# Performance work log

Hardware: AMD Instinct MI355X
Metric: run time of the kernel (lower is better)

Reference implementation:

```python
import jax, jax.numpy as jnp
import numpy as np


def _dwconv3x3(x, w, b):
    # depthwise 3x3, stride 1, padding 1 (groups == channels)
    y = jax.lax.conv_general_dilated(
        x, w, window_strides=(1, 1), padding=((1, 1), (1, 1)),
        dimension_numbers=('NCHW', 'OIHW', 'NCHW'),
        feature_group_count=x.shape[1])
    return y + b[None, :, None, None]


def _maxpool(x, f):
    # adaptive_max_pool2d to (h//f, w//f) with h,w divisible by f == stride-f max pool
    return jax.lax.reduce_window(x, -jnp.inf, jax.lax.max,
                                 (1, 1, f, f), (1, 1, f, f), 'VALID')


def _up_nearest(x, f):
    return jnp.repeat(jnp.repeat(x, f, axis=2), f, axis=3)


def setup_inputs() -> dict:
    key = jax.random.key(0)
    ks = jax.random.split(key, 10)
    B, C, H, W = 4, 32, 128, 128
    x = jax.random.normal(ks[0], (B, C, H, W), dtype=jnp.float32)
    mk = lambda k, shape, s: jax.random.normal(k, shape, dtype=jnp.float32) * s
    return {
        'x': x,
        'w0': mk(ks[1], (C, 1, 3, 3), 0.3), 'b0': mk(ks[2], (C,), 0.05),
        'w1': mk(ks[3], (C, 1, 3, 3), 0.3), 'b1': mk(ks[4], (C,), 0.05),
        'w2': mk(ks[5], (C, 1, 3, 3), 0.3), 'b2': mk(ks[6], (C,), 0.05),
        'wa': mk(ks[7], (C, C, 1, 1), 0.2), 'ba': mk(ks[8], (C,), 0.05),
    }


def reference(x, w0, b0, w1, b1, w2, b2, wa, ba):
    b, c, h, w = x.shape
    # multi-scale depthwise feature refinement
    s0 = _dwconv3x3(x, w0, b0)                               # level 0: full res
    s1 = _up_nearest(_dwconv3x3(_maxpool(x, 2), w1, b1), 2)  # level 1: /2
    s2 = _up_nearest(_dwconv3x3(_maxpool(x, 4), w2, b2), 4)  # level 2: /4
    # Channel_mixing8: q=s0, k=s1, v=s2; per-pixel CxC outer product
    to_nc = lambda t: t.transpose(0, 2, 3, 1).reshape(-1, c)  # (N, C), N=b*h*w
    q, k, v = to_nc(s0), to_nc(s1), to_nc(s2)
    kv = v[:, :, None] * k[:, None, :]        # (N, C, C) = v_embed @ k_embed^T
    attn = jax.nn.softmax(kv, axis=1)         # softmax over dim=1 (v axis)
    qkv = jnp.einsum('nij,nj->ni', attn, q)   # matvec with q
    out = qkv.reshape(b, h, w, c).transpose(0, 3, 1, 2)
    # aggr: 1x1 conv; drop_path=0 -> identity
    out = jnp.einsum('bchw,oc->bohw', out, wa[:, :, 0, 0]) + ba[None, :, None, None]
    return jax.nn.gelu(out, approximate=False) * x
```

## Files before the change

kernel.cpp:

```cpp
#include <hip/hip_runtime.h>
#include <math.h>

#define CC 32

__global__ __launch_bounds__(256, 2) void fused_safm(
    const float* __restrict__ x,
    const float* __restrict__ w0, const float* __restrict__ b0,
    const float* __restrict__ w1, const float* __restrict__ b1,
    const float* __restrict__ w2, const float* __restrict__ b2,
    const float* __restrict__ wa, const float* __restrict__ ba,
    float* __restrict__ out) {
  int bid = blockIdx.x;
  int tw = bid & 7;
  int th = (bid >> 3) & 63;
  int b  = bid >> 9;
  int t  = threadIdx.x;
  int h4  = th >> 1;
  int dth = (th & 1) * 2;
  int R0 = 4 * h4 - 4;
  int C0 = 16 * tw - 4;

  __shared__ __align__(16) float smA[11520];
  float* xs   = smA;
  float* p1s  = smA + 9600;
  float* p2s  = smA + 10848;
  float* Ebuf = smA;
  float* scT  = smA + 8288;
  __shared__ __align__(16) float s0s[1056];
  __shared__ __align__(16) float c1s[264];
  __shared__ __align__(16) float vsh[288];
  __shared__ __align__(16) float qkvs[1056];

  {
    int c = t >> 3, sub = t & 7;
    const float* xc = x + ((size_t)(b * CC + c) << 14);
    float* xd = xs + c * 300;
#pragma unroll
    for (int r = 0; r < 12; ++r) {
      int row = R0 + r;
      bool rok = (unsigned)row < 128u;
#pragma unroll
      for (int m = 0; m < 3; ++m) {
        int col = sub * 3 + m;
        int gcol = C0 + col;
        float v = 0.f;
        if (rok && (unsigned)gcol < 128u) v = xc[row * 128 + gcol];
        xd[r * 25 + col] = v;
      }
    }
  }
  __syncthreads();

  for (int k = 0; k < 4; ++k) {
    int idx = t + k * 256;
    if (idx < 960) {
      int c = idx / 30, rem = idx % 30;
      int hp = rem / 10, wp = rem % 10;
      int prow = th - 1 + hp, pcol = 8 * tw - 1 + wp;
      float v = 0.f;
      if ((unsigned)prow < 64u && (unsigned)pcol < 64u) {
        const float* xp = xs + c * 300 + (dth + 2 * hp + 2) * 25 + (2 * wp + 2);
        v = fmaxf(fmaxf(xp[0], xp[1]), fmaxf(xp[25], xp[26]));
      }
      p1s[c * 39 + hp * 13 + wp] = v;
    }
  }
  for (int k = 0; k < 3; ++k) {
    int idx = t + k * 256;
    if (idx < 576) {
      int c = idx / 18, rem = idx % 18;
      int hq = rem / 6, wq = rem % 6;
      int prow = h4 - 1 + hq, pcol = 4 * tw - 1 + wq;
      float v = 0.f;
      if ((unsigned)prow < 32u && (unsigned)pcol < 32u) {
        const float* xp = xs + c * 300 + (4 * hq) * 25 + 4 * wq;
        float m0 = fmaxf(fmaxf(xp[0],  xp[1]),  fmaxf(xp[2],  xp[3]));
        float m1 = fmaxf(fmaxf(xp[25], xp[26]), fmaxf(xp[27], xp[28]));
        float m2 = fmaxf(fmaxf(xp[50], xp[51]), fmaxf(xp[52], xp[53]));
        float m3 = fmaxf(fmaxf(xp[75], xp[76]), fmaxf(xp[77], xp[78]));
        v = fmaxf(fmaxf(m0, m1), fmaxf(m2, m3));
      }
      p2s[c * 21 + hq * 7 + wq] = v;
    }
  }
  __syncthreads();

  {
    int c = t >> 3, gg = t & 7;
    const float* wc = w0 + c * 9;
    float wv[9];
#pragma unroll
    for (int q = 0; q < 9; ++q) wv[q] = wc[q];
    float bz = b0[c];
    int hh = gg >> 2, wb = (gg & 3) * 4;
#pragma unroll
    for (int k = 0; k < 4; ++k) {
      int ww = wb + k;
      const float* xp = xs + c * 300 + (dth + hh + 3) * 25 + (ww + 3);
      float acc = bz;
      acc = fmaf(wv[0], xp[0],  fmaf(wv[1], xp[1],  fmaf(wv[2], xp[2],  acc)));
      acc = fmaf(wv[3], xp[25], fmaf(wv[4], xp[26], fmaf(wv[5], xp[27], acc)));
      acc = fmaf(wv[6], xp[50], fmaf(wv[7], xp[51], fmaf(wv[8], xp[52], acc)));
      s0s[(hh * 16 + ww) * 33 + c] = acc;
    }
  }
  {
    int eb = t >> 5, j = t & 31;
    {
      const float* wc = w1 + j * 9;
      const float* pp = p1s + j * 39 + eb;
      float acc = b1[j];
      acc = fmaf(wc[0], pp[0],  fmaf(wc[1], pp[1],  fmaf(wc[2], pp[2],  acc)));
      acc = fmaf(wc[3], pp[13], fmaf(wc[4], pp[14], fmaf(wc[5], pp[15], acc)));
      acc = fmaf(wc[6], pp[26], fmaf(wc[7], pp[27], fmaf(wc[8], pp[28], acc)));
      c1s[eb * 33 + j] = acc;
    }
    {
      const float* wc = w2 + j * 9;
      const float* pp = p2s + j * 21 + (eb >> 1);
      float acc = b2[j];
      acc = fmaf(wc[0], pp[0],  fmaf(wc[1], pp[1],  fmaf(wc[2], pp[2],  acc)));
      acc = fmaf(wc[3], pp[7],  fmaf(wc[4], pp[8],  fmaf(wc[5], pp[9],  acc)));
      acc = fmaf(wc[6], pp[14], fmaf(wc[7], pp[15], fmaf(wc[8], pp[16], acc)));
      vsh[eb * 36 + j] = acc;
    }
  }
  __syncthreads();

  {
    int eb = t >> 5, j = t & 31;
    float kj = c1s[eb * 33 + j];
    float vv[32];
    const float4* v4 = (const float4*)(vsh + eb * 36);
#pragma unroll
    for (int iq = 0; iq < 8; ++iq) {
      float4 q_ = v4[iq];
      vv[4 * iq] = q_.x; vv[4 * iq + 1] = q_.y; vv[4 * iq + 2] = q_.z; vv[4 * iq + 3] = q_.w;
    }
    float vmax = vv[0], vmin = vv[0];
#pragma unroll
    for (int i = 1; i < CC; ++i) {
      vmax = fmaxf(vmax, vv[i]);
      vmin = fminf(vmin, vv[i]);
    }
    const float L2E = 1.4426950408889634f;
    float m  = (kj >= 0.f) ? kj * vmax : kj * vmin;
    float kl = kj * L2E;
    float nm = -m * L2E;
    float d0 = 0.f, d1 = 0.f, d2 = 0.f, d3 = 0.f;
    float* Ecol = Ebuf + eb * 1036 + j;
#pragma unroll
    for (int i = 0; i < CC; i += 4) {
      float e0 = __builtin_amdgcn_exp2f(fmaf(vv[i],     kl, nm)); Ecol[i * 32]       = e0; d0 += e0;
      float e1 = __builtin_amdgcn_exp2f(fmaf(vv[i + 1], kl, nm)); Ecol[(i + 1) * 32] = e1; d1 += e1;
      float e2 = __builtin_amdgcn_exp2f(fmaf(vv[i + 2], kl, nm)); Ecol[(i + 2) * 32] = e2; d2 += e2;
      float e3 = __builtin_amdgcn_exp2f(fmaf(vv[i + 3], kl, nm)); Ecol[(i + 3) * 32] = e3; d3 += e3;
    }
    float rd = __fdividef(1.f, (d0 + d1) + (d2 + d3));
#pragma unroll
    for (int px = 0; px < 4; ++px) {
      int hh = px >> 1, wwb = px & 1;
      int p = hh * 16 + eb * 2 + wwb;
      scT[j * 33 + p] = s0s[p * 33 + j] * rd;
    }
  }
  __syncthreads();

  {
    int p = t & 31, ic = t >> 5;
    int eb = (p & 15) >> 1;
    const float* Er = Ebuf + eb * 1036 + ic * 128;
    float a0 = 0.f, a1 = 0.f, a2 = 0.f, a3 = 0.f;
#pragma unroll
    for (int jq = 0; jq < 8; ++jq) {
      float4 e0 = *(const float4*)(Er + jq * 4);
      float4 e1 = *(const float4*)(Er + 32 + jq * 4);
      float4 e2 = *(const float4*)(Er + 64 + jq * 4);
      float4 e3 = *(const float4*)(Er + 96 + jq * 4);
      float s0v = scT[(jq * 4)     * 33 + p];
      float s1v = scT[(jq * 4 + 1) * 33 + p];
      float s2v = scT[(jq * 4 + 2) * 33 + p];
      float s3v = scT[(jq * 4 + 3) * 33 + p];
      a0 = fmaf(e0.x, s0v, fmaf(e0.y, s1v, fmaf(e0.z, s2v, fmaf(e0.w, s3v, a0))));
      a1 = fmaf(e1.x, s0v, fmaf(e1.y, s1v, fmaf(e1.z, s2v, fmaf(e1.w, s3v, a1))));
      a2 = fmaf(e2.x, s0v, fmaf(e2.y, s1v, fmaf(e2.z, s2v, fmaf(e2.w, s3v, a2))));
      a3 = fmaf(e3.x, s0v, fmaf(e3.y, s1v, fmaf(e3.z, s2v, fmaf(e3.w, s3v, a3))));
    }
    int i0 = ic * 4;
    qkvs[p * 33 + i0]     = a0;
    qkvs[p * 33 + i0 + 1] = a1;
    qkvs[p * 33 + i0 + 2] = a2;
    qkvs[p * 33 + i0 + 3] = a3;
  }
  __syncthreads();

  {
    int o = t >> 3, g = t & 7;
    int hh = g >> 2, wb = (g & 3) * 4;
    const float* wo = wa + o * 32;
    const float* q0 = qkvs + (hh * 16 + wb)     * 33;
    const float* q1 = qkvs + (hh * 16 + wb + 1) * 33;
    const float* q2 = qkvs + (hh * 16 + wb + 2) * 33;
    const float* q3 = qkvs + (hh * 16 + wb + 3) * 33;
    float bz = ba[o];
    float y0 = bz, y1 = bz, y2 = bz, y3 = bz;
#pragma unroll
    for (int i = 0; i < 32; ++i) {
      float w = wo[i];
      y0 = fmaf(w, q0[i], y0);
      y1 = fmaf(w, q1[i], y1);
      y2 = fmaf(w, q2[i], y2);
      y3 = fmaf(w, q3[i], y3);
    }
    const float RS2 = 0.70710678118654752f;
    float g0 = 0.5f * y0 * (1.f + erff(y0 * RS2));
    float g1 = 0.5f * y1 * (1.f + erff(y1 * RS2));
    float g2 = 0.5f * y2 * (1.f + erff(y2 * RS2));
    float g3 = 0.5f * y3 * (1.f + erff(y3 * RS2));
    size_t ob = (((size_t)(b * CC + o) * 128) + (2 * th + hh)) * 128 + 16 * tw + wb;
    float4 xv = *(const float4*)(x + ob);
    float4 r;
    r.x = g0 * xv.x; r.y = g1 * xv.y; r.z = g2 * xv.z; r.w = g3 * xv.w;
    *(float4*)(out + ob) = r;
  }
}

extern "C" void kernel_launch(void* const* d_in, const int* in_sizes, int n_in,
                              void* d_out, int out_size, void* d_ws, size_t ws_size,
                              hipStream_t stream) {
  const float* x  = (const float*)d_in[0];
  const float* w0 = (const float*)d_in[1];
  const float* b0 = (const float*)d_in[2];
  const float* w1 = (const float*)d_in[3];
  const float* b1 = (const float*)d_in[4];
  const float* w2 = (const float*)d_in[5];
  const float* b2 = (const float*)d_in[6];
  const float* wa = (const float*)d_in[7];
  const float* ba = (const float*)d_in[8];
  float* out = (float*)d_out;

  fused_safm<<<2048, 256, 0, stream>>>(x, w0, b0, w1, b1, w2, b2, wa, ba, out);
}
```

Before: 120.5 us.

## Drop shared x tile, derive pool4 from pool2, store softmax weights as fp16

Stops staging the 12x25 input halo tile per channel in shared memory. Level-1 pooling now reads x straight from global with float2 loads, the full-res depthwise conv reads x rows directly, and level-2 pooling is taken as the max over the level-1 pool buffer. The normalized softmax weights are packed to half2 in shared memory and the matvec reads them as fp16 pairs, and the launch-bounds occupancy hint rises from 2 to 5 blocks. This shrinks LDS use and one barrier to allow more resident blocks, at the cost of more, partly redundant, global loads and fp16 rounding of the attention weights.

```diff
diff --git a/kernel.cpp b/kernel.cpp
--- a/kernel.cpp
+++ b/kernel.cpp
@@ -1,9 +1,18 @@
 #include <hip/hip_runtime.h>
+#include <hip/hip_fp16.h>
 #include <math.h>
 
-#define CC 32
-
-__global__ __launch_bounds__(256, 2) void fused_safm(
+
+__device__ __forceinline__ float2 h2f2(unsigned int u) {
+  __half2 h = *reinterpret_cast<__half2*>(&u);
+  return __half22float2(h);
+}
+__device__ __forceinline__ unsigned int f2h2(float a, float b) {
+  __half2 h = __floats2half2_rn(a, b);
+  return *reinterpret_cast<unsigned int*>(&h);
+}
+
+__global__ __launch_bounds__(256, 5) void fused_safm(
     const float* __restrict__ x,
     const float* __restrict__ w0, const float* __restrict__ b0,
     const float* __restrict__ w1, const float* __restrict__ b1,
@@ -11,127 +20,99 @@
     const float* __restrict__ wa, const float* __restrict__ ba,
     float* __restrict__ out) {
   int bid = blockIdx.x;
-  int tw = bid & 7;
-  int th = (bid >> 3) & 63;
-  int b  = bid >> 9;
-  int t  = threadIdx.x;
-  int h4  = th >> 1;
-  int dth = (th & 1) * 2;
-  int R0 = 4 * h4 - 4;
-  int C0 = 16 * tw - 4;
-
-  __shared__ __align__(16) float smA[11520];
-  float* xs   = smA;
-  float* p1s  = smA + 9600;
-  float* p2s  = smA + 10848;
-  float* Ebuf = smA;
-  float* scT  = smA + 8288;
+  int tw = bid & 7, th = (bid >> 3) & 63, b = bid >> 9;
+  int t = threadIdx.x;
+  int h4 = th >> 1;
+
+  __shared__ __align__(16) unsigned int regA[4128];
   __shared__ __align__(16) float s0s[1056];
-  __shared__ __align__(16) float c1s[264];
   __shared__ __align__(16) float vsh[288];
   __shared__ __align__(16) float qkvs[1056];
-
-  {
-    int c = t >> 3, sub = t & 7;
-    const float* xc = x + ((size_t)(b * CC + c) << 14);
-    float* xd = xs + c * 300;
-#pragma unroll
-    for (int r = 0; r < 12; ++r) {
-      int row = R0 + r;
-      bool rok = (unsigned)row < 128u;
-#pragma unroll
-      for (int m = 0; m < 3; ++m) {
-        int col = sub * 3 + m;
-        int gcol = C0 + col;
-        float v = 0.f;
-        if (rok && (unsigned)gcol < 128u) v = xc[row * 128 + gcol];
-        xd[r * 25 + col] = v;
+  float* p1s = (float*)regA;
+
+  {
+#pragma unroll
+    for (int kk = 0; kk < 9; ++kk) {
+      int idx = t + kk * 256;
+      int c = idx / 72, rem = idx % 72;
+      int r = rem / 12, w = rem % 12;
+      int pr = 2 * h4 - 2 + r, pc = 8 * tw - 2 + w;
+      float v = 0.f;
+      if ((unsigned)pr < 64u && (unsigned)pc < 64u) {
+        const float* xp = x + ((size_t)(b * 32 + c) << 14) + 2 * pr * 128 + 2 * pc;
+        float2 r0 = *(const float2*)xp;
+        float2 r1 = *(const float2*)(xp + 128);
+        v = fmaxf(fmaxf(r0.x, r0.y), fmaxf(r1.x, r1.y));
       }
-    }
-  }
-  __syncthreads();
-
-  for (int k = 0; k < 4; ++k) {
-    int idx = t + k * 256;
-    if (idx < 960) {
-      int c = idx / 30, rem = idx % 30;
-      int hp = rem / 10, wp = rem % 10;
-      int prow = th - 1 + hp, pcol = 8 * tw - 1 + wp;
-      float v = 0.f;
-      if ((unsigned)prow < 64u && (unsigned)pcol < 64u) {
-        const float* xp = xs + c * 300 + (dth + 2 * hp + 2) * 25 + (2 * wp + 2);
-        v = fmaxf(fmaxf(xp[0], xp[1]), fmaxf(xp[25], xp[26]));
-      }
-      p1s[c * 39 + hp * 13 + wp] = v;
-    }
-  }
-  for (int k = 0; k < 3; ++k) {
-    int idx = t + k * 256;
-    if (idx < 576) {
-      int c = idx / 18, rem = idx % 18;
-      int hq = rem / 6, wq = rem % 6;
-      int prow = h4 - 1 + hq, pcol = 4 * tw - 1 + wq;
-      float v = 0.f;
-      if ((unsigned)prow < 32u && (unsigned)pcol < 32u) {
-        const float* xp = xs + c * 300 + (4 * hq) * 25 + 4 * wq;
-        float m0 = fmaxf(fmaxf(xp[0],  xp[1]),  fmaxf(xp[2],  xp[3]));
-        float m1 = fmaxf(fmaxf(xp[25], xp[26]), fmaxf(xp[27], xp[28]));
-        float m2 = fmaxf(fmaxf(xp[50], xp[51]), fmaxf(xp[52], xp[53]));
-        float m3 = fmaxf(fmaxf(xp[75], xp[76]), fmaxf(xp[77], xp[78]));
-        v = fmaxf(fmaxf(m0, m1), fmaxf(m2, m3));
-      }
-      p2s[c * 21 + hq * 7 + wq] = v;
-    }
-  }
-  __syncthreads();
-
+      p1s[c * 73 + r * 12 + w] = v;
+    }
+  }
   {
     int c = t >> 3, gg = t & 7;
+    int hh = gg >> 2, wb = (gg & 3) * 4;
+    const float* xp = x + ((size_t)(b * 32 + c) << 14);
     const float* wc = w0 + c * 9;
     float wv[9];
 #pragma unroll
     for (int q = 0; q < 9; ++q) wv[q] = wc[q];
     float bz = b0[c];
-    int hh = gg >> 2, wb = (gg & 3) * 4;
-#pragma unroll
-    for (int k = 0; k < 4; ++k) {
-      int ww = wb + k;
-      const float* xp = xs + c * 300 + (dth + hh + 3) * 25 + (ww + 3);
-      float acc = bz;
-      acc = fmaf(wv[0], xp[0],  fmaf(wv[1], xp[1],  fmaf(wv[2], xp[2],  acc)));
-      acc = fmaf(wv[3], xp[25], fmaf(wv[4], xp[26], fmaf(wv[5], xp[27], acc)));
-      acc = fmaf(wv[6], xp[50], fmaf(wv[7], xp[51], fmaf(wv[8], xp[52], acc)));
-      s0s[(hh * 16 + ww) * 33 + c] = acc;
-    }
-  }
-  {
-    int eb = t >> 5, j = t & 31;
-    {
-      const float* wc = w1 + j * 9;
-      const float* pp = p1s + j * 39 + eb;
-      float acc = b1[j];
-      acc = fmaf(wc[0], pp[0],  fmaf(wc[1], pp[1],  fmaf(wc[2], pp[2],  acc)));
-      acc = fmaf(wc[3], pp[13], fmaf(wc[4], pp[14], fmaf(wc[5], pp[15], acc)));
-      acc = fmaf(wc[6], pp[26], fmaf(wc[7], pp[27], fmaf(wc[8], pp[28], acc)));
-      c1s[eb * 33 + j] = acc;
-    }
-    {
-      const float* wc = w2 + j * 9;
-      const float* pp = p2s + j * 21 + (eb >> 1);
-      float acc = b2[j];
-      acc = fmaf(wc[0], pp[0],  fmaf(wc[1], pp[1],  fmaf(wc[2], pp[2],  acc)));
-      acc = fmaf(wc[3], pp[7],  fmaf(wc[4], pp[8],  fmaf(wc[5], pp[9],  acc)));
-      acc = fmaf(wc[6], pp[14], fmaf(wc[7], pp[15], fmaf(wc[8], pp[16], acc)));
-      vsh[eb * 36 + j] = acc;
-    }
-  }
-  __syncthreads();
-
-  {
-    int eb = t >> 5, j = t & 31;
-    float kj = c1s[eb * 33 + j];
+    float a0 = bz, a1 = bz, a2 = bz, a3 = bz;
+    int cbase = 16 * tw + wb;
+#pragma unroll
+    for (int dr = -1; dr <= 1; ++dr) {
+      int row = 2 * th + hh + dr;
+      if ((unsigned)row >= 128u) continue;
+      const float* rp = xp + row * 128 + cbase;
+      float cm1 = (cbase > 0)       ? rp[-1] : 0.f;
+      float4 c03 = *(const float4*)rp;
+      float c4  = (cbase + 4 < 128) ? rp[4]  : 0.f;
+      float wA = wv[(dr + 1) * 3], wB = wv[(dr + 1) * 3 + 1], wC = wv[(dr + 1) * 3 + 2];
+      a0 = fmaf(wA, cm1,   fmaf(wB, c03.x, fmaf(wC, c03.y, a0)));
+      a1 = fmaf(wA, c03.x, fmaf(wB, c03.y, fmaf(wC, c03.z, a1)));
+      a2 = fmaf(wA, c03.y, fmaf(wB, c03.z, fmaf(wC, c03.w, a2)));
+      a3 = fmaf(wA, c03.z, fmaf(wB, c03.w, fmaf(wC, c4,    a3)));
+    }
+    int pb = hh * 16 + wb;
+    s0s[(pb)     * 33 + c] = a0;
+    s0s[(pb + 1) * 33 + c] = a1;
+    s0s[(pb + 2) * 33 + c] = a2;
+    s0s[(pb + 3) * 33 + c] = a3;
+  }
+  __syncthreads();
+
+  int ebT = t >> 5, jT = t & 31;
+  float kreg;
+  {
+    const float* wc = w1 + jT * 9;
+    const float* Pk = p1s + jT * 73 + ((th & 1) + 1) * 12 + ebT + 1;
+    float acc = b1[jT];
+    acc = fmaf(wc[0], Pk[0],  fmaf(wc[1], Pk[1],  fmaf(wc[2], Pk[2],  acc)));
+    acc = fmaf(wc[3], Pk[12], fmaf(wc[4], Pk[13], fmaf(wc[5], Pk[14], acc)));
+    acc = fmaf(wc[6], Pk[24], fmaf(wc[7], Pk[25], fmaf(wc[8], Pk[26], acc)));
+    kreg = acc;
+  }
+  {
+    const float* wc = w2 + jT * 9;
+    const float* P = p1s + jT * 73;
+    int cb0 = 2 * (ebT >> 1);
+    float acc = b2[jT];
+#pragma unroll
+    for (int hq = 0; hq < 3; ++hq) {
+      const float* Pr = P + 2 * hq * 12;
+#pragma unroll
+      for (int wq = 0; wq < 3; ++wq) {
+        int cb = cb0 + 2 * wq;
+        float p2v = fmaxf(fmaxf(Pr[cb], Pr[cb + 1]), fmaxf(Pr[cb + 12], Pr[cb + 13]));
+        acc = fmaf(wc[hq * 3 + wq], p2v, acc);
+      }
+    }
+    vsh[ebT * 36 + jT] = acc;
+  }
+  __syncthreads();
+
+  {
     float vv[32];
-    const float4* v4 = (const float4*)(vsh + eb * 36);
+    const float4* v4 = (const float4*)(vsh + ebT * 36);
 #pragma unroll
     for (int iq = 0; iq < 8; ++iq) {
       float4 q_ = v4[iq];
@@ -139,58 +120,55 @@
     }
     float vmax = vv[0], vmin = vv[0];
 #pragma unroll
-    for (int i = 1; i < CC; ++i) {
+    for (int i = 1; i < 32; ++i) {
       vmax = fmaxf(vmax, vv[i]);
       vmin = fminf(vmin, vv[i]);
     }
     const float L2E = 1.4426950408889634f;
-    float m  = (kj >= 0.f) ? kj * vmax : kj * vmin;
-    float kl = kj * L2E;
+    float m  = (kreg >= 0.f) ? kreg * vmax : kreg * vmin;
+    float kl = kreg * L2E;
     float nm = -m * L2E;
+    float e[32];
     float d0 = 0.f, d1 = 0.f, d2 = 0.f, d3 = 0.f;
-    float* Ecol = Ebuf + eb * 1036 + j;
-#pragma unroll
-    for (int i = 0; i < CC; i += 4) {
-      float e0 = __builtin_amdgcn_exp2f(fmaf(vv[i],     kl, nm)); Ecol[i * 32]       = e0; d0 += e0;
-      float e1 = __builtin_amdgcn_exp2f(fmaf(vv[i + 1], kl, nm)); Ecol[(i + 1) * 32] = e1; d1 += e1;
-      float e2 = __builtin_amdgcn_exp2f(fmaf(vv[i + 2], kl, nm)); Ecol[(i + 2) * 32] = e2; d2 += e2;
-      float e3 = __builtin_amdgcn_exp2f(fmaf(vv[i + 3], kl, nm)); Ecol[(i + 3) * 32] = e3; d3 += e3;
+#pragma unroll
+    for (int i = 0; i < 32; i += 4) {
+      e[i]     = __builtin_amdgcn_exp2f(fmaf(vv[i],     kl, nm)); d0 += e[i];
+      e[i + 1] = __builtin_amdgcn_exp2f(fmaf(vv[i + 1], kl, nm)); d1 += e[i + 1];
+      e[i + 2] = __builtin_amdgcn_exp2f(fmaf(vv[i + 2], kl, nm)); d2 += e[i + 2];
+      e[i + 3] = __builtin_amdgcn_exp2f(fmaf(vv[i + 3], kl, nm)); d3 += e[i + 3];
     }
     float rd = __fdividef(1.f, (d0 + d1) + (d2 + d3));
-#pragma unroll
-    for (int px = 0; px < 4; ++px) {
-      int hh = px >> 1, wwb = px & 1;
-      int p = hh * 16 + eb * 2 + wwb;
-      scT[j * 33 + p] = s0s[p * 33 + j] * rd;
-    }
+    unsigned int* EB = regA + ebT * 516 + jT;
+#pragma unroll
+    for (int ip = 0; ip < 16; ++ip)
+      EB[ip * 32] = f2h2(e[2 * ip] * rd, e[2 * ip + 1] * rd);
   }
   __syncthreads();
 
   {
     int p = t & 31, ic = t >> 5;
     int eb = (p & 15) >> 1;
-    const float* Er = Ebuf + eb * 1036 + ic * 128;
+    const unsigned int* EB = regA + eb * 516;
+    const float* qrow = s0s + p * 33;
     float a0 = 0.f, a1 = 0.f, a2 = 0.f, a3 = 0.f;
 #pragma unroll
-    for (int jq = 0; jq < 8; ++jq) {
-      float4 e0 = *(const float4*)(Er + jq * 4);
-      float4 e1 = *(const float4*)(Er + 32 + jq * 4);
-      float4 e2 = *(const float4*)(Er + 64 + jq * 4);
-      float4 e3 = *(const float4*)(Er + 96 + jq * 4);
-      float s0v = scT[(jq * 4)     * 33 + p];
-      float s1v = scT[(jq * 4 + 1) * 33 + p];
-      float s2v = scT[(jq * 4 + 2) * 33 + p];
-      float s3v = scT[(jq * 4 + 3) * 33 + p];
-      a0 = fmaf(e0.x, s0v, fmaf(e0.y, s1v, fmaf(e0.z, s2v, fmaf(e0.w, s3v, a0))));
-      a1 = fmaf(e1.x, s0v, fmaf(e1.y, s1v, fmaf(e1.z, s2v, fmaf(e1.w, s3v, a1))));
-      a2 = fmaf(e2.x, s0v, fmaf(e2.y, s1v, fmaf(e2.z, s2v, fmaf(e2.w, s3v, a2))));
-      a3 = fmaf(e3.x, s0v, fmaf(e3.y, s1v, fmaf(e3.z, s2v, fmaf(e3.w, s3v, a3))));
-    }
-    int i0 = ic * 4;
-    qkvs[p * 33 + i0]     = a0;
-    qkvs[p * 33 + i0 + 1] = a1;
-    qkvs[p * 33 + i0 + 2] = a2;
-    qkvs[p * 33 + i0 + 3] = a3;
+    for (int jw = 0; jw < 8; ++jw) {
+      uint4 wA = *(const uint4*)(EB + (2 * ic)     * 32 + jw * 4);
+      uint4 wB = *(const uint4*)(EB + (2 * ic + 1) * 32 + jw * 4);
+      float q0 = qrow[4 * jw], q1 = qrow[4 * jw + 1];
+      float q2 = qrow[4 * jw + 2], q3 = qrow[4 * jw + 3];
+      float2 f;
+      f = h2f2(wA.x); a0 = fmaf(f.x, q0, a0); a1 = fmaf(f.y, q0, a1);
+      f = h2f2(wA.y); a0 = fmaf(f.x, q1, a0); a1 = fmaf(f.y, q1, a1);
+      f = h2f2(wA.z); a0 = fmaf(f.x, q2, a0); a1 = fmaf(f.y, q2, a1);
+      f = h2f2(wA.w); a0 = fmaf(f.x, q3, a0); a1 = fmaf(f.y, q3, a1);
+      f = h2f2(wB.x); a2 = fmaf(f.x, q0, a2); a3 = fmaf(f.y, q0, a3);
+      f = h2f2(wB.y); a2 = fmaf(f.x, q1, a2); a3 = fmaf(f.y, q1, a3);
+      f = h2f2(wB.z); a2 = fmaf(f.x, q2, a2); a3 = fmaf(f.y, q2, a3);
+      f = h2f2(wB.w); a2 = fmaf(f.x, q3, a2); a3 = fmaf(f.y, q3, a3);
+    }
+    float* qd = qkvs + p * 33 + ic * 4;
+    qd[0] = a0; qd[1] = a1; qd[2] = a2; qd[3] = a3;
   }
   __syncthreads();
 
@@ -217,7 +195,7 @@
     float g1 = 0.5f * y1 * (1.f + erff(y1 * RS2));
     float g2 = 0.5f * y2 * (1.f + erff(y2 * RS2));
     float g3 = 0.5f * y3 * (1.f + erff(y3 * RS2));
-    size_t ob = (((size_t)(b * CC + o) * 128) + (2 * th + hh)) * 128 + 16 * tw + wb;
+    size_t ob = (((size_t)(b * 32 + o) * 128) + (2 * th + hh)) * 128 + 16 * tw + wb;
     float4 xv = *(const float4*)(x + ob);
     float4 r;
     r.x = g0 * xv.x; r.y = g1 * xv.y; r.z = g2 * xv.z; r.w = g3 * xv.w;
```

Result: slower. 144.9 us (+20.3%).
